# Kernel optimization log

Hardware: AMD Instinct MI355X
Metric: run time of the kernel (lower is better)

## Reference

```python
import jax, jax.numpy as jnp
import numpy as np
import math

B, S, H = 2, 2048, 2048
NH = 16
HD = H // NH  # 128
ROPE_THETA = 10000.0


def setup_inputs() -> dict:
    key = jax.random.key(0)
    kx, kq, kk, kv, ko = jax.random.split(key, 5)
    x = jax.random.normal(kx, (B, S, H), jnp.float32)
    # standard llama RoPE tables: angles[p, j] = p / theta^(2j/HD)
    inv_freq = 1.0 / (ROPE_THETA ** (jnp.arange(0, HD, 2, dtype=jnp.float32) / HD))
    ang = jnp.arange(S, dtype=jnp.float32)[:, None] * inv_freq[None, :]  # [S, HD/2]
    scale = 1.0 / math.sqrt(H)
    return {
        "input_tensor": x,
        "freqs_cos": jnp.cos(ang),
        "freqs_sin": jnp.sin(ang),
        "padding_mask": jnp.ones((B, S), jnp.int32),
        "Wq": jax.random.normal(kq, (H, H), jnp.float32) * scale,
        "Wk": jax.random.normal(kk, (H, H), jnp.float32) * scale,
        "Wv": jax.random.normal(kv, (H, H), jnp.float32) * scale,
        "Wo": jax.random.normal(ko, (H, H), jnp.float32) * scale,
    }


def _apply_rope(t, cos, sin):
    # t: [b, s, h, d]; rotate consecutive pairs (complex multiply)
    b, s, h, d = t.shape
    t2 = t.reshape(b, s, h, d // 2, 2)
    c = cos[None, :, None, :]  # [1, s, 1, d/2]
    sn = sin[None, :, None, :]
    re = t2[..., 0] * c - t2[..., 1] * sn
    im = t2[..., 0] * sn + t2[..., 1] * c
    return jnp.stack([re, im], axis=-1).reshape(b, s, h, d)


def reference(input_tensor, freqs_cos, freqs_sin, padding_mask, Wq, Wk, Wv, Wo):
    b, s, _ = input_tensor.shape
    # torch nn.Linear: y = x @ W.T (weight stored [out, in])
    q = (input_tensor @ Wq.T).reshape(b, s, NH, HD)
    k = (input_tensor @ Wk.T).reshape(b, s, NH, HD)
    v = (input_tensor @ Wv.T).reshape(b, s, NH, HD)
    q = _apply_rope(q, freqs_cos, freqs_sin)
    k = _apply_rope(k, freqs_cos, freqs_sin)
    q = q.transpose(0, 2, 1, 3)  # b h s d
    k = k.transpose(0, 2, 1, 3)
    v = v.transpose(0, 2, 1, 3)
    scores = jnp.einsum('bhsd,bhtd->bhst', q, k) / math.sqrt(HD)
    pad = jnp.where(padding_mask.astype(bool), 0.0, -10000.0).astype(scores.dtype)
    scores = scores + pad[:, None, None, :]
    causal = jnp.where(jnp.tril(jnp.ones((s, s), bool)), 0.0, -1e9).astype(scores.dtype)
    scores = scores + causal[None, None, :, :]
    attn = jax.nn.softmax(scores.astype(jnp.float32), axis=-1).astype(q.dtype)
    out = jnp.einsum('bhst,bhtd->bhsd', attn, v)
    out = out.transpose(0, 2, 1, 3).reshape(b, s, NH * HD)
    return out @ Wo.T
```

## Files before the change

### kernel.cpp

```cpp
#include <hip/hip_runtime.h>
#include <math.h>

#define Bn  2
#define Sn  2048
#define Hn  2048
#define NHn 16
#define HDn 128
#define Mn  (Bn * Sn)
#define Kd  Hn

typedef __attribute__((ext_vector_type(8))) short bf16x8;
typedef __attribute__((ext_vector_type(4))) float fx4;

__device__ __forceinline__ unsigned short f2bf(float f) {
    union { float f; unsigned u; } v; v.f = f;
    unsigned r = v.u + 0x7fffu + ((v.u >> 16) & 1u);
    return (unsigned short)(r >> 16);
}

__device__ __forceinline__ void gload16(const unsigned short* g, unsigned short* l) {
    __builtin_amdgcn_global_load_lds(
        (const __attribute__((address_space(1))) unsigned int*)g,
        (__attribute__((address_space(3))) unsigned int*)l, 16, 0, 0);
}

__device__ __forceinline__ fx4 mfma16(bf16x8 a, bf16x8 b, fx4 c) {
    return __builtin_amdgcn_mfma_f32_16x16x32_bf16(a, b, c, 0, 0, 0);
}

__global__ __launch_bounds__(256)
void cvt_kernel(const float* __restrict__ src, unsigned short* __restrict__ dst, int n8)
{
    int i = blockIdx.x * 256 + threadIdx.x;
    if (i >= n8) return;
    const float4* s = (const float4*)src + (size_t)i * 2;
    float4 a = s[0], b = s[1];
    bf16x8 o;
    o[0] = (short)f2bf(a.x); o[1] = (short)f2bf(a.y);
    o[2] = (short)f2bf(a.z); o[3] = (short)f2bf(a.w);
    o[4] = (short)f2bf(b.x); o[5] = (short)f2bf(b.y);
    o[6] = (short)f2bf(b.z); o[7] = (short)f2bf(b.w);
    *(bf16x8*)(dst + (size_t)i * 8) = o;
}

__global__ __launch_bounds__(256)
void cvt4_kernel(const float* __restrict__ w0, const float* __restrict__ w1,
                 const float* __restrict__ w2, const float* __restrict__ w3,
                 unsigned short* __restrict__ d0, unsigned short* __restrict__ d1,
                 unsigned short* __restrict__ d2, unsigned short* __restrict__ d3,
                 int n8)
{
    int i = blockIdx.x * 256 + threadIdx.x;
    if (i >= n8) return;
    const float* w = (blockIdx.y == 0) ? w0 : (blockIdx.y == 1) ? w1
                    : (blockIdx.y == 2) ? w2 : w3;
    unsigned short* d = (blockIdx.y == 0) ? d0 : (blockIdx.y == 1) ? d1
                       : (blockIdx.y == 2) ? d2 : d3;
    const float4* s = (const float4*)w + (size_t)i * 2;
    float4 a = s[0], b = s[1];
    bf16x8 o;
    o[0] = (short)f2bf(a.x); o[1] = (short)f2bf(a.y);
    o[2] = (short)f2bf(a.z); o[3] = (short)f2bf(a.w);
    o[4] = (short)f2bf(b.x); o[5] = (short)f2bf(b.y);
    o[6] = (short)f2bf(b.z); o[7] = (short)f2bf(b.w);
    *(bf16x8*)(d + (size_t)i * 8) = o;
}

#define HALF_SH 8192
#define B_BASE  32768

__device__ __forceinline__ void gemm256(const unsigned short* __restrict__ A,
                                        const unsigned short* __restrict__ W,
                                        int m0, int n0, fx4 acc[8][4],
                                        unsigned short* smem)
{
    const int t = threadIdx.x;
    const int wid = t >> 6, lane = t & 63;
    const int wm = wid >> 2, wn = wid & 3;
    const int lr = lane & 15, lg = lane >> 4;
    const int swr = ((lr >> 2) & 3) << 4;

    const int row0 = t >> 3,         row1 = (t + 512) >> 3;
    const int gc0 = ((t & 7) * 8) ^ (((row0 >> 2) & 3) << 4);
    const int gc1 = ((t & 7) * 8) ^ (((row1 >> 2) & 3) << 4);
    const unsigned short* Ag[2][2];
    const unsigned short* Bg[2][2];
    Ag[0][0] = A + (size_t)(m0 + row0) * Kd + gc0;
    Ag[0][1] = A + (size_t)(m0 + row1) * Kd + gc1;
    Ag[1][0] = A + (size_t)(m0 + 128 + row0) * Kd + gc0;
    Ag[1][1] = A + (size_t)(m0 + 128 + row1) * Kd + gc1;
    Bg[0][0] = W + (size_t)(n0 + row0) * Kd + gc0;
    Bg[0][1] = W + (size_t)(n0 + row1) * Kd + gc1;
    Bg[1][0] = W + (size_t)(n0 + 128 + row0) * Kd + gc0;
    Bg[1][1] = W + (size_t)(n0 + 128 + row1) * Kd + gc1;
    const int dst0 = wid * 512;
    const int dst1 = wid * 512 + 4096;

    bf16x8 aM[4][2], bLo[2][2], bHi[2][2];

    auto STAGE_A = [&](int buf, int koff) {
        gload16(Ag[0][0] + koff, smem + (buf * 2 + 0) * HALF_SH + dst0);
        gload16(Ag[0][1] + koff, smem + (buf * 2 + 0) * HALF_SH + dst1);
        gload16(Ag[1][0] + koff, smem + (buf * 2 + 1) * HALF_SH + dst0);
        gload16(Ag[1][1] + koff, smem + (buf * 2 + 1) * HALF_SH + dst1);
    };
    auto STAGE_B = [&](int buf, int koff) {
        gload16(Bg[0][0] + koff, smem + B_BASE + (buf * 2 + 0) * HALF_SH + dst0);
        gload16(Bg[0][1] + koff, smem + B_BASE + (buf * 2 + 0) * HALF_SH + dst1);
        gload16(Bg[1][0] + koff, smem + B_BASE + (buf * 2 + 1) * HALF_SH + dst0);
        gload16(Bg[1][1] + koff, smem + B_BASE + (buf * 2 + 1) * HALF_SH + dst1);
    };
    auto LDA = [&](int buf, int milo) {
        const unsigned short* base = smem + (buf * 2 + wm) * HALF_SH;
        #pragma unroll
        for (int i = 0; i < 4; ++i) {
            int rl = (milo + i) * 16 + lr;
            #pragma unroll
            for (int kk = 0; kk < 2; ++kk)
                aM[i][kk] = *(const bf16x8*)(base + rl * 64 + ((kk * 32 + lg * 8) ^ swr));
        }
    };
    auto LDB = [&](int buf, int njlo, bf16x8 (&br)[2][2]) {
        const unsigned short* base = smem + B_BASE + (buf * 2 + (wn >> 1)) * HALF_SH;
        #pragma unroll
        for (int j = 0; j < 2; ++j) {
            int rl = (wn & 1) * 64 + (njlo + j) * 16 + lr;
            #pragma unroll
            for (int kk = 0; kk < 2; ++kk)
                br[j][kk] = *(const bf16x8*)(base + rl * 64 + ((kk * 32 + lg * 8) ^ swr));
        }
    };
    auto MM = [&](int milo, int njlo, bf16x8 (&br)[2][2]) {
        __builtin_amdgcn_s_setprio(1);
        #pragma unroll
        for (int i = 0; i < 4; ++i)
            #pragma unroll
            for (int j = 0; j < 2; ++j)
                #pragma unroll
                for (int kk = 0; kk < 2; ++kk)
                    acc[milo + i][njlo + j] =
                        mfma16(aM[i][kk], br[j][kk], acc[milo + i][njlo + j]);
        __builtin_amdgcn_s_setprio(0);
    };

    STAGE_A(0, 0);
    STAGE_B(0, 0);
    asm volatile("s_waitcnt vmcnt(0)" ::: "memory");
    __builtin_amdgcn_s_barrier();

    const int NT = Kd / 64;
    for (int tk = 0; tk < NT; ++tk) {
        const int cur = tk & 1, nxt = cur ^ 1;
        const int koff = (tk + 1) * 64;
        if (tk + 1 < NT) STAGE_A(nxt, koff);
        LDA(cur, 0);
        LDB(cur, 0, bLo);
        __builtin_amdgcn_s_barrier();
        MM(0, 0, bLo);
        __builtin_amdgcn_s_barrier();
        if (tk + 1 < NT) STAGE_B(nxt, koff);
        LDB(cur, 2, bHi);
        __builtin_amdgcn_s_barrier();
        MM(0, 2, bHi);
        __builtin_amdgcn_s_barrier();
        LDA(cur, 4);
        __builtin_amdgcn_s_barrier();
        MM(4, 2, bHi);
        __builtin_amdgcn_s_barrier();
        MM(4, 0, bLo);
        asm volatile("s_waitcnt vmcnt(0)" ::: "memory");
        __builtin_amdgcn_s_barrier();
    }
}

__global__ __launch_bounds__(512, 2)
void qkv_kernel(const unsigned short* __restrict__ xb,
                const unsigned short* __restrict__ wq, const unsigned short* __restrict__ wk,
                const unsigned short* __restrict__ wv,
                const float* __restrict__ fcos, const float* __restrict__ fsin,
                unsigned short* __restrict__ qb, unsigned short* __restrict__ kb,
                unsigned short* __restrict__ vtb)
{
    extern __shared__ unsigned short smem[];
    const int mode = blockIdx.z;
    const unsigned short* W = (mode == 0) ? wq : (mode == 1) ? wk : wv;
    const int m0 = blockIdx.x * 256, n0 = blockIdx.y * 256;

    fx4 zero = {0.f, 0.f, 0.f, 0.f};
    fx4 acc[8][4];
    #pragma unroll
    for (int i = 0; i < 8; ++i)
        #pragma unroll
        for (int j = 0; j < 4; ++j) acc[i][j] = zero;

    gemm256(xb, W, m0, n0, acc, smem);

    const int t = threadIdx.x, wid = t >> 6, lane = t & 63;
    const int wm = wid >> 2, wn = wid & 3, lr = lane & 15, lg = lane >> 4;
    if (mode < 2) {
        unsigned short* outp = (mode == 0) ? qb : kb;
        #pragma unroll
        for (int mi = 0; mi < 8; ++mi) {
            int mbase = m0 + wm * 128 + mi * 16 + lg * 4;
            #pragma unroll
            for (int nj = 0; nj < 4; ++nj) {
                int ncol = n0 + wn * 64 + nj * 16 + lr;
                int h = ncol >> 7, dh = ncol & 127;
                #pragma unroll
                for (int r = 0; r < 4; ++r) {
                    int m = mbase + r, b = m >> 11, s = m & (Sn - 1);
                    float vv = acc[mi][nj][r];
                    float other = __shfl_xor(vv, 1, 64);
                    float c  = fcos[s * (HDn / 2) + (dh >> 1)];
                    float sn = fsin[s * (HDn / 2) + (dh >> 1)];
                    float res = (dh & 1) ? (other * sn + vv * c) : (vv * c - other * sn);
                    outp[(((size_t)b * NHn + h) * Sn + s) * HDn + dh] = f2bf(res);
                }
            }
        }
    } else {
        #pragma unroll
        for (int mi = 0; mi < 8; ++mi) {
            int mbase = m0 + wm * 128 + mi * 16 + lg * 4;
            int b = mbase >> 11, s = mbase & (Sn - 1);
            #pragma unroll
            for (int nj = 0; nj < 4; ++nj) {
                int ncol = n0 + wn * 64 + nj * 16 + lr;
                int h = ncol >> 7, dh = ncol & 127;
                ushort4 pk;
                pk.x = f2bf(acc[mi][nj][0]); pk.y = f2bf(acc[mi][nj][1]);
                pk.z = f2bf(acc[mi][nj][2]); pk.w = f2bf(acc[mi][nj][3]);
                *(ushort4*)(vtb + (((size_t)b * NHn + h) * HDn + dh) * Sn + s) = pk;
            }
        }
    }
}

__global__ __launch_bounds__(512, 2)
void oproj_kernel(const unsigned short* __restrict__ attnb,
                  const unsigned short* __restrict__ wob, float* __restrict__ out)
{
    extern __shared__ unsigned short smem[];
    const int m0 = blockIdx.x * 256, n0 = blockIdx.y * 256;
    fx4 zero = {0.f, 0.f, 0.f, 0.f};
    fx4 acc[8][4];
    #pragma unroll
    for (int i = 0; i < 8; ++i)
        #pragma unroll
        for (int j = 0; j < 4; ++j) acc[i][j] = zero;

    gemm256(attnb, wob, m0, n0, acc, smem);

    const int t = threadIdx.x, wid = t >> 6, lane = t & 63;
    const int wm = wid >> 2, wn = wid & 3, lr = lane & 15, lg = lane >> 4;
    #pragma unroll
    for (int mi = 0; mi < 8; ++mi) {
        #pragma unroll
        for (int r = 0; r < 4; ++r) {
            int m = m0 + wm * 128 + mi * 16 + lg * 4 + r;
            #pragma unroll
            for (int nj = 0; nj < 4; ++nj)
                out[(size_t)m * Hn + n0 + wn * 64 + nj * 16 + lr] = acc[mi][nj][r];
        }
    }
}

#define KROW 136
#define VROW 72
#define PROW 68

__global__ __launch_bounds__(256)
void attn_kernel(const unsigned short* __restrict__ qb,
                 const unsigned short* __restrict__ kb,
                 const unsigned short* __restrict__ vtb,
                 const int* __restrict__ pmask, unsigned short* __restrict__ attnb)
{
    __shared__ unsigned short Ksl[64 * KROW];
    __shared__ unsigned short Vsl[128 * VROW];
    __shared__ unsigned short Psl[4 * 16 * PROW];

    const int pr = blockIdx.x, h = blockIdx.y, b = blockIdx.z;
    const size_t base = ((size_t)b * NHn + h) * Sn * HDn;
    const unsigned short* Qp = qb + base;
    const unsigned short* Kp = kb + base;
    const unsigned short* Vt = vtb + base;
    const int t = threadIdx.x, w = t >> 6, lane = t & 63;
    const int lr = lane & 15, lg = lane >> 4;
    const float scale = 0.08838834764831845f;
    fx4 zero = {0.f, 0.f, 0.f, 0.f};

    for (int ph = 0; ph < 2; ++ph) {
        const int qt = ph ? (31 - pr) : pr;
        const int q0 = qt * 64;
        const int nt = qt + 1;

        bf16x8 qf[4];
        #pragma unroll
        for (int kf = 0; kf < 4; ++kf)
            qf[kf] = *(const bf16x8*)(Qp + (size_t)(q0 + w * 16 + lr) * HDn + kf * 32 + lg * 8);

        fx4 oacc[8];
        #pragma unroll
        for (int j = 0; j < 8; ++j) oacc[j] = zero;
        float mrow[4] = {-1e30f, -1e30f, -1e30f, -1e30f};
        float lsum[4] = {0.f, 0.f, 0.f, 0.f};

        bf16x8 kreg[4], vreg[4];
        #pragma unroll
        for (int q = 0; q < 4; ++q) {
            int chunk = t + q * 256, row = chunk >> 4, c = chunk & 15;
            kreg[q] = *(const bf16x8*)(Kp + (size_t)row * HDn + c * 8);
        }
        #pragma unroll
        for (int q = 0; q < 4; ++q) {
            int chunk = t + q * 256, row = chunk >> 3, c = chunk & 7;
            vreg[q] = *(const bf16x8*)(Vt + (size_t)row * Sn + c * 8);
        }

        for (int kt = 0; kt < nt; ++kt) {
            const int kv0 = kt * 64;
            __syncthreads();
            #pragma unroll
            for (int q = 0; q < 4; ++q) {
                int chunk = t + q * 256, row = chunk >> 4, c = chunk & 15;
                *(bf16x8*)(Ksl + row * KROW + c * 8) = kreg[q];
            }
            #pragma unroll
            for (int q = 0; q < 4; ++q) {
                int chunk = t + q * 256, row = chunk >> 3, c = chunk & 7;
                *(bf16x8*)(Vsl + row * VROW + c * 8) = vreg[q];
            }
            __syncthreads();
            if (kt + 1 < nt) {
                #pragma unroll
                for (int q = 0; q < 4; ++q) {
                    int chunk = t + q * 256, row = chunk >> 4, c = chunk & 15;
                    kreg[q] = *(const bf16x8*)(Kp + (size_t)(kv0 + 64 + row) * HDn + c * 8);
                }
                #pragma unroll
                for (int q = 0; q < 4; ++q) {
                    int chunk = t + q * 256, row = chunk >> 3, c = chunk & 7;
                    vreg[q] = *(const bf16x8*)(Vt + (size_t)row * Sn + kv0 + 64 + c * 8);
                }
            }

            fx4 sc[4];
            __builtin_amdgcn_s_setprio(1);
            #pragma unroll
            for (int nf = 0; nf < 4; ++nf) {
                fx4 z = zero;
                #pragma unroll
                for (int kf = 0; kf < 4; ++kf) {
                    bf16x8 kfr = *(const bf16x8*)(Ksl + (nf * 16 + lr) * KROW + kf * 32 + lg * 8);
                    z = __builtin_amdgcn_mfma_f32_16x16x32_bf16(qf[kf], kfr, z, 0, 0, 0);
                }
                sc[nf] = z;
            }
            __builtin_amdgcn_s_setprio(0);

            float pmv[4];
            #pragma unroll
            for (int nf = 0; nf < 4; ++nf)
                pmv[nf] = pmask[b * Sn + kv0 + nf * 16 + lr] ? 0.f : -10000.f;
            float tmax[4];
            #pragma unroll
            for (int r = 0; r < 4; ++r) {
                int qrow = q0 + w * 16 + lg * 4 + r;
                float mx = -1e30f;
                #pragma unroll
                for (int nf = 0; nf < 4; ++nf) {
                    int kg = kv0 + nf * 16 + lr;
                    float v = sc[nf][r] * scale + pmv[nf] + ((kg > qrow) ? -1e9f : 0.f);
                    sc[nf][r] = v;
                    mx = fmaxf(mx, v);
                }
                tmax[r] = mx;
            }
            #pragma unroll
            for (int off = 1; off < 16; off <<= 1)
                #pragma unroll
                for (int r = 0; r < 4; ++r)
                    tmax[r] = fmaxf(tmax[r], __shfl_xor(tmax[r], off, 64));
            float grow = 0.f;
            #pragma unroll
            for (int r = 0; r < 4; ++r) grow = fmaxf(grow, tmax[r] - mrow[r]);
            if (__any(grow > 8.f)) {
                #pragma unroll
                for (int r = 0; r < 4; ++r) {
                    float mnew = fmaxf(mrow[r], tmax[r]);
                    float sf = __expf(mrow[r] - mnew);
                    mrow[r] = mnew;
                    lsum[r] *= sf;
                    #pragma unroll
                    for (int j = 0; j < 8; ++j) oacc[j][r] *= sf;
                }
            }
            float psum[4];
            #pragma unroll
            for (int r = 0; r < 4; ++r) {
                float ps = 0.f;
                #pragma unroll
                for (int nf = 0; nf < 4; ++nf) {
                    float p = __expf(sc[nf][r] - mrow[r]);
                    sc[nf][r] = p;
                    ps += p;
                }
                psum[r] = ps;
            }
            #pragma unroll
            for (int off = 1; off < 16; off <<= 1)
                #pragma unroll
                for (int r = 0; r < 4; ++r)
                    psum[r] += __shfl_xor(psum[r], off, 64);
            #pragma unroll
            for (int r = 0; r < 4; ++r) lsum[r] += psum[r];

            unsigned short* Pw = Psl + w * 16 * PROW;
            #pragma unroll
            for (int nf = 0; nf < 4; ++nf)
                #pragma unroll
                for (int r = 0; r < 4; ++r)
                    Pw[(lg * 4 + r) * PROW + nf * 16 + lr] = f2bf(sc[nf][r]);
            __builtin_amdgcn_s_setprio(1);
            #pragma unroll
            for (int kf2 = 0; kf2 < 2; ++kf2) {
                bf16x8 pf = *(const bf16x8*)(Pw + lr * PROW + kf2 * 32 + lg * 8);
                #pragma unroll
                for (int j = 0; j < 8; ++j) {
                    bf16x8 vf = *(const bf16x8*)(Vsl + (j * 16 + lr) * VROW + kf2 * 32 + lg * 8);
                    oacc[j] = __builtin_amdgcn_mfma_f32_16x16x32_bf16(pf, vf, oacc[j], 0, 0, 0);
                }
            }
            __builtin_amdgcn_s_setprio(0);
        }

        #pragma unroll
        for (int j = 0; j < 8; ++j) {
            int d = j * 16 + lr;
            #pragma unroll
            for (int r = 0; r < 4; ++r) {
                int s = q0 + w * 16 + lg * 4 + r;
                attnb[((size_t)b * Sn + s) * Hn + h * HDn + d] = f2bf(oacc[j][r] / lsum[r]);
            }
        }
        __syncthreads();
    }
}

extern "C" void kernel_launch(void* const* d_in, const int* in_sizes, int n_in,
                              void* d_out, int out_size, void* d_ws, size_t ws_size,
                              hipStream_t stream)
{
    const float* x     = (const float*)d_in[0];
    const float* fcos  = (const float*)d_in[1];
    const float* fsin  = (const float*)d_in[2];
    const int*   pmask = (const int*)d_in[3];
    const float* Wq    = (const float*)d_in[4];
    const float* Wk    = (const float*)d_in[5];
    const float* Wv    = (const float*)d_in[6];
    const float* Wo    = (const float*)d_in[7];
    float* out = (float*)d_out;
    (void)in_sizes; (void)n_in; (void)out_size; (void)ws_size;

    const size_t NX = (size_t)Mn * Hn;
    const size_t NW = (size_t)Hn * Hn;
    unsigned short* xb   = (unsigned short*)d_ws;
    unsigned short* wqb  = xb  + NX;
    unsigned short* wkb  = wqb + NW;
    unsigned short* wvb  = wkb + NW;
    unsigned short* wob  = wvb + NW;
    unsigned short* qb   = wob + NW;
    unsigned short* kb   = qb  + NX;
    unsigned short* vtb  = kb  + NX;
    unsigned short* attnb= vtb + NX;

    const int GEMM_LDS = 131072;
    hipFuncSetAttribute((const void*)qkv_kernel,
                        hipFuncAttributeMaxDynamicSharedMemorySize, GEMM_LDS);
    hipFuncSetAttribute((const void*)oproj_kernel,
                        hipFuncAttributeMaxDynamicSharedMemorySize, GEMM_LDS);

    cvt_kernel<<<dim3((int)(NX / 8 / 256)), 256, 0, stream>>>(x, xb, (int)(NX / 8));
    cvt4_kernel<<<dim3((int)(NW / 8 / 256), 4), 256, 0, stream>>>(
        Wq, Wk, Wv, Wo, wqb, wkb, wvb, wob, (int)(NW / 8));
    qkv_kernel<<<dim3(Mn / 256, Hn / 256, 3), 512, GEMM_LDS, stream>>>(
        xb, wqb, wkb, wvb, fcos, fsin, qb, kb, vtb);
    attn_kernel<<<dim3(16, NHn, Bn), 256, 0, stream>>>(qb, kb, vtb, pmask, attnb);
    oproj_kernel<<<dim3(Mn / 256, Hn / 256), 512, GEMM_LDS, stream>>>(attnb, wob, out);
}
```

Measured before the change: 452.4 us.

## Rework GEMM prefetch and swizzle, fold Q scale, simplify softmax, shrink O-proj tiles

The 256x256 GEMM now uses an 8-way XOR swizzle and splits the A-tile loads into early and late halves, with partial vmcnt waits so global loads overlap more with MFMA work. The softmax scale is folded into Q at the RoPE epilogue. The attention kernel applies the causal mask only on diagonal tiles, reduces the row max across lanes only when a rescale is needed, and defers the row-sum shuffle reduction to the end. The output projection switches to a simpler 128x128 single-buffered GEMM with static LDS, trading software pipelining for more blocks. The lazy max check now compares per-lane maxima before reduction, and the changed swizzle has to match between the load and read sides.

Result: faster. 422.2 us (-6.7%).

```diff
diff --git a/kernel.cpp b/kernel.cpp
--- a/kernel.cpp
+++ b/kernel.cpp
@@ -78,38 +78,39 @@
     const int wid = t >> 6, lane = t & 63;
     const int wm = wid >> 2, wn = wid & 3;
     const int lr = lane & 15, lg = lane >> 4;
-    const int swr = ((lr >> 2) & 3) << 4;
-
-    const int row0 = t >> 3,         row1 = (t + 512) >> 3;
-    const int gc0 = ((t & 7) * 8) ^ (((row0 >> 2) & 3) << 4);
-    const int gc1 = ((t & 7) * 8) ^ (((row1 >> 2) & 3) << 4);
+    const int swr = ((lr >> 1) & 7) << 3;
+
+    const int row0 = t >> 3;
+    const int gcs  = ((t & 7) * 8) ^ (((t >> 4) & 7) << 3);
     const unsigned short* Ag[2][2];
     const unsigned short* Bg[2][2];
-    Ag[0][0] = A + (size_t)(m0 + row0) * Kd + gc0;
-    Ag[0][1] = A + (size_t)(m0 + row1) * Kd + gc1;
-    Ag[1][0] = A + (size_t)(m0 + 128 + row0) * Kd + gc0;
-    Ag[1][1] = A + (size_t)(m0 + 128 + row1) * Kd + gc1;
-    Bg[0][0] = W + (size_t)(n0 + row0) * Kd + gc0;
-    Bg[0][1] = W + (size_t)(n0 + row1) * Kd + gc1;
-    Bg[1][0] = W + (size_t)(n0 + 128 + row0) * Kd + gc0;
-    Bg[1][1] = W + (size_t)(n0 + 128 + row1) * Kd + gc1;
+    Ag[0][0] = A + (size_t)(m0 + row0) * Kd + gcs;
+    Ag[0][1] = A + (size_t)(m0 + row0 + 64) * Kd + gcs;
+    Ag[1][0] = A + (size_t)(m0 + 128 + row0) * Kd + gcs;
+    Ag[1][1] = A + (size_t)(m0 + 128 + row0 + 64) * Kd + gcs;
+    Bg[0][0] = W + (size_t)(n0 + row0) * Kd + gcs;
+    Bg[0][1] = W + (size_t)(n0 + row0 + 64) * Kd + gcs;
+    Bg[1][0] = W + (size_t)(n0 + 128 + row0) * Kd + gcs;
+    Bg[1][1] = W + (size_t)(n0 + 128 + row0 + 64) * Kd + gcs;
     const int dst0 = wid * 512;
     const int dst1 = wid * 512 + 4096;
 
     bf16x8 aM[4][2], bLo[2][2], bHi[2][2];
 
-    auto STAGE_A = [&](int buf, int koff) {
+    auto ISSUE_A_EARLY = [&](int buf, int koff) {
         gload16(Ag[0][0] + koff, smem + (buf * 2 + 0) * HALF_SH + dst0);
-        gload16(Ag[0][1] + koff, smem + (buf * 2 + 0) * HALF_SH + dst1);
         gload16(Ag[1][0] + koff, smem + (buf * 2 + 1) * HALF_SH + dst0);
-        gload16(Ag[1][1] + koff, smem + (buf * 2 + 1) * HALF_SH + dst1);
     };
-    auto STAGE_B = [&](int buf, int koff) {
+    auto ISSUE_B = [&](int buf, int koff) {
         gload16(Bg[0][0] + koff, smem + B_BASE + (buf * 2 + 0) * HALF_SH + dst0);
         gload16(Bg[0][1] + koff, smem + B_BASE + (buf * 2 + 0) * HALF_SH + dst1);
         gload16(Bg[1][0] + koff, smem + B_BASE + (buf * 2 + 1) * HALF_SH + dst0);
         gload16(Bg[1][1] + koff, smem + B_BASE + (buf * 2 + 1) * HALF_SH + dst1);
     };
+    auto ISSUE_A_LATE = [&](int buf, int koff) {
+        gload16(Ag[0][1] + koff, smem + (buf * 2 + 0) * HALF_SH + dst1);
+        gload16(Ag[1][1] + koff, smem + (buf * 2 + 1) * HALF_SH + dst1);
+    };
     auto LDA = [&](int buf, int milo) {
         const unsigned short* base = smem + (buf * 2 + wm) * HALF_SH;
         #pragma unroll
@@ -143,32 +144,37 @@
         __builtin_amdgcn_s_setprio(0);
     };
 
-    STAGE_A(0, 0);
-    STAGE_B(0, 0);
-    asm volatile("s_waitcnt vmcnt(0)" ::: "memory");
+    ISSUE_A_EARLY(0, 0);
+    ISSUE_B(0, 0);
+    ISSUE_A_LATE(0, 0);
+    asm volatile("s_waitcnt vmcnt(2)" ::: "memory");
     __builtin_amdgcn_s_barrier();
 
     const int NT = Kd / 64;
     for (int tk = 0; tk < NT; ++tk) {
         const int cur = tk & 1, nxt = cur ^ 1;
         const int koff = (tk + 1) * 64;
-        if (tk + 1 < NT) STAGE_A(nxt, koff);
+        const bool more = (tk + 1 < NT);
+        if (more) ISSUE_A_EARLY(nxt, koff);
         LDA(cur, 0);
         LDB(cur, 0, bLo);
         __builtin_amdgcn_s_barrier();
         MM(0, 0, bLo);
         __builtin_amdgcn_s_barrier();
-        if (tk + 1 < NT) STAGE_B(nxt, koff);
+        if (more) ISSUE_B(nxt, koff);
         LDB(cur, 2, bHi);
         __builtin_amdgcn_s_barrier();
         MM(0, 2, bHi);
-        __builtin_amdgcn_s_barrier();
+        if (more) { asm volatile("s_waitcnt vmcnt(6)" ::: "memory"); }
+        else      { asm volatile("s_waitcnt vmcnt(0)" ::: "memory"); }
+        __builtin_amdgcn_s_barrier();
+        if (more) ISSUE_A_LATE(nxt, koff);
         LDA(cur, 4);
         __builtin_amdgcn_s_barrier();
         MM(4, 2, bHi);
         __builtin_amdgcn_s_barrier();
         MM(4, 0, bLo);
-        asm volatile("s_waitcnt vmcnt(0)" ::: "memory");
+        asm volatile("s_waitcnt vmcnt(2)" ::: "memory");
         __builtin_amdgcn_s_barrier();
     }
 }
@@ -199,6 +205,7 @@
     const int wm = wid >> 2, wn = wid & 3, lr = lane & 15, lg = lane >> 4;
     if (mode < 2) {
         unsigned short* outp = (mode == 0) ? qb : kb;
+        const float qsc = (mode == 0) ? 0.08838834764831845f : 1.0f;
         #pragma unroll
         for (int mi = 0; mi < 8; ++mi) {
             int mbase = m0 + wm * 128 + mi * 16 + lg * 4;
@@ -214,7 +221,7 @@
                     float c  = fcos[s * (HDn / 2) + (dh >> 1)];
                     float sn = fsin[s * (HDn / 2) + (dh >> 1)];
                     float res = (dh & 1) ? (other * sn + vv * c) : (vv * c - other * sn);
-                    outp[(((size_t)b * NHn + h) * Sn + s) * HDn + dh] = f2bf(res);
+                    outp[(((size_t)b * NHn + h) * Sn + s) * HDn + dh] = f2bf(res * qsc);
                 }
             }
         }
@@ -236,31 +243,76 @@
     }
 }
 
-__global__ __launch_bounds__(512, 2)
+__device__ __forceinline__ void gemm_mfma(const unsigned short* __restrict__ A,
+                                          const unsigned short* __restrict__ W,
+                                          int m0, int n0, fx4 acc[4][4],
+                                          unsigned short* Asl, unsigned short* Bsl)
+{
+    const int t = threadIdx.x;
+    const int w = t >> 6, lane = t & 63;
+    const int wm = w >> 1, wn = w & 1;
+    const int lr = lane & 15, lg = lane >> 4;
+
+    const int srow = w * 32 + (lane >> 2);
+    const int scol = (lane & 3) * 8;
+    const unsigned short* Ag0 = A + (size_t)(m0 + srow) * Kd + scol;
+    const unsigned short* Ag1 = Ag0 + (size_t)16 * Kd;
+    const unsigned short* Bg0 = W + (size_t)(n0 + srow) * Kd + scol;
+    const unsigned short* Bg1 = Bg0 + (size_t)16 * Kd;
+    unsigned short* Ad0 = Asl + w * 1024;
+    unsigned short* Ad1 = Asl + w * 1024 + 512;
+    unsigned short* Bd0 = Bsl + w * 1024;
+    unsigned short* Bd1 = Bsl + w * 1024 + 512;
+
+    for (int k0 = 0; k0 < Kd; k0 += 32) {
+        __syncthreads();
+        gload16(Ag0 + k0, Ad0);
+        gload16(Ag1 + k0, Ad1);
+        gload16(Bg0 + k0, Bd0);
+        gload16(Bg1 + k0, Bd1);
+        __syncthreads();
+
+        bf16x8 af[4], bfr[4];
+        #pragma unroll
+        for (int i = 0; i < 4; ++i)
+            af[i] = *(const bf16x8*)(Asl + (wm * 64 + i * 16 + lr) * 32 + lg * 8);
+        #pragma unroll
+        for (int j = 0; j < 4; ++j)
+            bfr[j] = *(const bf16x8*)(Bsl + (wn * 64 + j * 16 + lr) * 32 + lg * 8);
+        #pragma unroll
+        for (int i = 0; i < 4; ++i)
+            #pragma unroll
+            for (int j = 0; j < 4; ++j)
+                acc[i][j] = mfma16(af[i], bfr[j], acc[i][j]);
+    }
+}
+
+__global__ __launch_bounds__(256)
 void oproj_kernel(const unsigned short* __restrict__ attnb,
                   const unsigned short* __restrict__ wob, float* __restrict__ out)
 {
-    extern __shared__ unsigned short smem[];
-    const int m0 = blockIdx.x * 256, n0 = blockIdx.y * 256;
+    __shared__ unsigned short Asl[128 * 32];
+    __shared__ unsigned short Bsl[128 * 32];
+    const int m0 = blockIdx.x * 128, n0 = blockIdx.y * 128;
     fx4 zero = {0.f, 0.f, 0.f, 0.f};
-    fx4 acc[8][4];
+    fx4 acc[4][4];
     #pragma unroll
-    for (int i = 0; i < 8; ++i)
+    for (int i = 0; i < 4; ++i)
         #pragma unroll
         for (int j = 0; j < 4; ++j) acc[i][j] = zero;
 
-    gemm256(attnb, wob, m0, n0, acc, smem);
-
-    const int t = threadIdx.x, wid = t >> 6, lane = t & 63;
-    const int wm = wid >> 2, wn = wid & 3, lr = lane & 15, lg = lane >> 4;
+    gemm_mfma(attnb, wob, m0, n0, acc, Asl, Bsl);
+
+    const int t = threadIdx.x, w = t >> 6, lane = t & 63;
+    const int wm = w >> 1, wn = w & 1, lr = lane & 15, lg = lane >> 4;
     #pragma unroll
-    for (int mi = 0; mi < 8; ++mi) {
+    for (int i = 0; i < 4; ++i) {
         #pragma unroll
         for (int r = 0; r < 4; ++r) {
-            int m = m0 + wm * 128 + mi * 16 + lg * 4 + r;
-            #pragma unroll
-            for (int nj = 0; nj < 4; ++nj)
-                out[(size_t)m * Hn + n0 + wn * 64 + nj * 16 + lr] = acc[mi][nj][r];
+            int m = m0 + wm * 64 + i * 16 + lg * 4 + r;
+            #pragma unroll
+            for (int j = 0; j < 4; ++j)
+                out[(size_t)m * Hn + n0 + wn * 64 + j * 16 + lr] = acc[i][j][r];
         }
     }
 }
@@ -286,7 +338,6 @@
     const unsigned short* Vt = vtb + base;
     const int t = threadIdx.x, w = t >> 6, lane = t & 63;
     const int lr = lane & 15, lg = lane >> 4;
-    const float scale = 0.08838834764831845f;
     fx4 zero = {0.f, 0.f, 0.f, 0.f};
 
     for (int ph = 0; ph < 2; ++ph) {
@@ -362,6 +413,7 @@
             #pragma unroll
             for (int nf = 0; nf < 4; ++nf)
                 pmv[nf] = pmask[b * Sn + kv0 + nf * 16 + lr] ? 0.f : -10000.f;
+            const bool diag = (kt == qt);
             float tmax[4];
             #pragma unroll
             for (int r = 0; r < 4; ++r) {
@@ -369,22 +421,22 @@
                 float mx = -1e30f;
                 #pragma unroll
                 for (int nf = 0; nf < 4; ++nf) {
-                    int kg = kv0 + nf * 16 + lr;
-                    float v = sc[nf][r] * scale + pmv[nf] + ((kg > qrow) ? -1e9f : 0.f);
+                    float v = sc[nf][r] + pmv[nf];
+                    if (diag && (kv0 + nf * 16 + lr > qrow)) v = -1e9f;
                     sc[nf][r] = v;
                     mx = fmaxf(mx, v);
                 }
                 tmax[r] = mx;
             }
-            #pragma unroll
-            for (int off = 1; off < 16; off <<= 1)
-                #pragma unroll
-                for (int r = 0; r < 4; ++r)
-                    tmax[r] = fmaxf(tmax[r], __shfl_xor(tmax[r], off, 64));
-            float grow = 0.f;
-            #pragma unroll
-            for (int r = 0; r < 4; ++r) grow = fmaxf(grow, tmax[r] - mrow[r]);
-            if (__any(grow > 8.f)) {
+            bool need = false;
+            #pragma unroll
+            for (int r = 0; r < 4; ++r) need = need || (tmax[r] > mrow[r] + 8.f);
+            if (__any(need)) {
+                #pragma unroll
+                for (int off = 1; off < 16; off <<= 1)
+                    #pragma unroll
+                    for (int r = 0; r < 4; ++r)
+                        tmax[r] = fmaxf(tmax[r], __shfl_xor(tmax[r], off, 64));
                 #pragma unroll
                 for (int r = 0; r < 4; ++r) {
                     float mnew = fmaxf(mrow[r], tmax[r]);
@@ -395,7 +447,6 @@
                     for (int j = 0; j < 8; ++j) oacc[j][r] *= sf;
                 }
             }
-            float psum[4];
             #pragma unroll
             for (int r = 0; r < 4; ++r) {
                 float ps = 0.f;
@@ -405,15 +456,8 @@
                     sc[nf][r] = p;
                     ps += p;
                 }
-                psum[r] = ps;
-            }
-            #pragma unroll
-            for (int off = 1; off < 16; off <<= 1)
-                #pragma unroll
-                for (int r = 0; r < 4; ++r)
-                    psum[r] += __shfl_xor(psum[r], off, 64);
-            #pragma unroll
-            for (int r = 0; r < 4; ++r) lsum[r] += psum[r];
+                lsum[r] += ps;
+            }
 
             unsigned short* Pw = Psl + w * 16 * PROW;
             #pragma unroll
@@ -433,6 +477,12 @@
             }
             __builtin_amdgcn_s_setprio(0);
         }
+
+        #pragma unroll
+        for (int off = 1; off < 16; off <<= 1)
+            #pragma unroll
+            for (int r = 0; r < 4; ++r)
+                lsum[r] += __shfl_xor(lsum[r], off, 64);
 
         #pragma unroll
         for (int j = 0; j < 8; ++j) {
@@ -477,8 +527,6 @@
     const int GEMM_LDS = 131072;
     hipFuncSetAttribute((const void*)qkv_kernel,
                         hipFuncAttributeMaxDynamicSharedMemorySize, GEMM_LDS);
-    hipFuncSetAttribute((const void*)oproj_kernel,
-                        hipFuncAttributeMaxDynamicSharedMemorySize, GEMM_LDS);
 
     cvt_kernel<<<dim3((int)(NX / 8 / 256)), 256, 0, stream>>>(x, xb, (int)(NX / 8));
     cvt4_kernel<<<dim3((int)(NW / 8 / 256), 4), 256, 0, stream>>>(
@@ -486,5 +534,5 @@
     qkv_kernel<<<dim3(Mn / 256, Hn / 256, 3), 512, GEMM_LDS, stream>>>(
         xb, wqb, wkb, wvb, fcos, fsin, qb, kb, vtb);
     attn_kernel<<<dim3(16, NHn, Bn), 256, 0, stream>>>(qb, kb, vtb, pmask, attnb);
-    oproj_kernel<<<dim3(Mn / 256, Hn / 256), 512, GEMM_LDS, stream>>>(attnb, wob, out);
-}
+    oproj_kernel<<<dim3(Mn / 128, Hn / 128), 256, 0, stream>>>(attnb, wob, out);
+}
```
